# Performance work log

Measured on AMD Instinct MI355X. Metric: run time of the kernel, lower is better.

## Reference

```python
import jax, jax.numpy as jnp
import numpy as np

NOT_EPSILON = 1.0
W_SCALE = 0.05  # scaled randn init for numerical stability of swishmax logits

H, T, A, C = 8, 1024, 64, 256  # heads, key/query size, attention size, compress size


def swishmax(x, axis):
    m = jnp.max(x, axis=axis, keepdims=True)
    xe = x * jnp.exp(x - m)
    return xe / (jnp.sum(jnp.abs(xe), axis=axis, keepdims=True) + NOT_EPSILON)


def setup_inputs() -> dict:
    key = jax.random.key(0)
    ks = jax.random.split(key, 7)
    B, Q, K = 2, 2048, 2048
    return {
        "query_tokens": jax.random.normal(ks[0], (B, Q, T), dtype=jnp.float32),
        "key_tokens": jax.random.normal(ks[1], (B, K, T), dtype=jnp.float32),
        "key_down": jax.random.normal(ks[2], (H, T, A), dtype=jnp.float32) * W_SCALE,
        "query_down": jax.random.normal(ks[3], (H, T, A), dtype=jnp.float32) * W_SCALE,
        "query_down_bias": jax.random.normal(ks[4], (H, 1, A), dtype=jnp.float32) * W_SCALE,
        "value_down": jax.random.normal(ks[5], (H, T, C), dtype=jnp.float32) * W_SCALE,
        "value_up": jax.random.normal(ks[6], (H, C, T), dtype=jnp.float32) * W_SCALE,
    }


def reference(query_tokens, key_tokens, key_down, query_down, query_down_bias, value_down, value_up):
    # key/query projections: [B,K,T] x [H,T,A] -> [B,H,K,A]
    k = jnp.einsum('bkt,hta->bhka', key_tokens, key_down)
    q = jnp.einsum('bqt,hta->bhqa', query_tokens, query_down) + query_down_bias[None]  # [B,H,Q,A]
    # attention logits: key @ query^T -> [B,H,K,Q]
    logits = jnp.einsum('bhka,bhqa->bhkq', k, q)
    attn = swishmax(logits, axis=-2)  # normalized over keys (dim=-2)
    # sum_k key_tokens[b,k,:] * attn[b,h,k,q]  ==  [B,H,Q,T] (matmul form of the outer-product sum)
    vs = jnp.einsum('bhkq,bkt->bhqt', attn, key_tokens)
    # compress path: value_down then value_up
    vs = jnp.einsum('bhqc,hct->bhqt', jnp.einsum('bhqt,htc->bhqc', vs, value_down), value_up)
    return vs.sum(axis=1)  # sum over heads -> [B,Q,T]
```

## Files before the change

kernel.cpp:

```cpp
#include <hip/hip_runtime.h>
#include <hip/hip_fp16.h>
#include <math.h>


typedef _Float16 f16;
typedef _Float16 f16x4 __attribute__((ext_vector_type(4)));
typedef _Float16 f16x8 __attribute__((ext_vector_type(8)));
typedef short s16x4 __attribute__((ext_vector_type(4)));
typedef short bf16x8 __attribute__((ext_vector_type(8)));
typedef float f32x4 __attribute__((ext_vector_type(4)));

#define MFMA_F16(a, b, c) __builtin_amdgcn_mfma_f32_16x16x32_f16(a, b, c, 0, 0, 0)
#define MFMA_BF16(a, b, c) __builtin_amdgcn_mfma_f32_16x16x32_bf16(a, b, c, 0, 0, 0)

__device__ __forceinline__ void g2lds16(const void* g, void* l) {
  __builtin_amdgcn_global_load_lds((__attribute__((address_space(1))) void*)g,
                                   (__attribute__((address_space(3))) void*)l, 16, 0, 0);
}

__device__ __forceinline__ short f32_bf16(float x) {
  union { float f; unsigned u; } v; v.f = x;
  unsigned r = v.u + 0x7FFFu + ((v.u >> 16) & 1u);
  return (short)(r >> 16);
}
__device__ __forceinline__ float bf16_f32(short h) {
  union { unsigned u; float f; } v; v.u = ((unsigned)(unsigned short)h) << 16;
  return v.f;
}

__global__ __launch_bounds__(256) void ew_split2(const float* __restrict__ qin,
                                                 const float* __restrict__ kin,
                                                 short* __restrict__ qhi,
                                                 short* __restrict__ qlo,
                                                 short* __restrict__ khi,
                                                 short* __restrict__ klo,
                                                 f16* __restrict__ kf) {
  int i = blockIdx.x * 256 + threadIdx.x;
  const bool isK = i >= 1048576;
  const int j = isK ? i - 1048576 : i;
  const float* in = isK ? kin : qin;
  f32x4 v = ((const f32x4*)in)[j];
  s16x4 h, l;
  f16x4 f;
#pragma unroll
  for (int e = 0; e < 4; e++) {
    short he = f32_bf16(v[e]);
    h[e] = he;
    l[e] = f32_bf16(v[e] - bf16_f32(he));
    f[e] = (f16)v[e];
  }
  if (isK) {
    ((s16x4*)khi)[j] = h;
    ((s16x4*)klo)[j] = l;
    ((f16x4*)kf)[j] = f;
  } else {
    ((s16x4*)qhi)[j] = h;
    ((s16x4*)qlo)[j] = l;
  }
}

__global__ __launch_bounds__(256) void transpose_all(
    const float* __restrict__ qdw, const float* __restrict__ kdw,
    const float* __restrict__ vdw, const float* __restrict__ vup,
    short* __restrict__ wqT_hi, short* __restrict__ wqT_lo,
    short* __restrict__ wkT_hi, short* __restrict__ wkT_lo,
    f16* __restrict__ vdT, f16* __restrict__ vuT) {
  __shared__ float t[64][65];
  int idx = blockIdx.x;
  const float* in;
  short *bhi = nullptr, *blo = nullptr;
  f16* fo = nullptr;
  int R, C, cb, rb;
  size_t batch;
  if (idx < 256) {
    bool isQ = idx < 128;
    int i = isQ ? idx : idx - 128;
    in = isQ ? qdw : kdw;
    bhi = isQ ? wqT_hi : wkT_hi;
    blo = isQ ? wqT_lo : wkT_lo;
    R = 1024; C = 64; cb = 0; rb = (i & 15) * 64;
    batch = (size_t)(i >> 4) * R * C;
  } else if (idx < 768) {
    int i = idx - 256;
    in = vdw; fo = vdT;
    R = 1024; C = 256; cb = (i & 3) * 64; rb = ((i >> 2) & 15) * 64;
    batch = (size_t)(i >> 6) * R * C;
  } else {
    int i = idx - 768;
    in = vup; fo = vuT;
    R = 2048; C = 1024; cb = (i & 15) * 64; rb = (i >> 4) * 64;
    batch = 0;
  }
  int tid = threadIdx.x;
#pragma unroll
  for (int i = 0; i < 4; i++) {
    int r = (tid >> 4) + i * 16, c4 = (tid & 15) * 4;
    f32x4 v = *(const f32x4*)(in + batch + (size_t)(rb + r) * C + cb + c4);
    t[r][c4] = v[0]; t[r][c4 + 1] = v[1]; t[r][c4 + 2] = v[2]; t[r][c4 + 3] = v[3];
  }
  __syncthreads();
#pragma unroll
  for (int i = 0; i < 4; i++) {
    int c = (tid >> 4) + i * 16, r4 = (tid & 15) * 4;
    float v0 = t[r4][c], v1 = t[r4 + 1][c], v2 = t[r4 + 2][c], v3 = t[r4 + 3][c];
    size_t o = batch + (size_t)(cb + c) * R + rb + r4;
    if (bhi) {
      s16x4 h = {f32_bf16(v0), f32_bf16(v1), f32_bf16(v2), f32_bf16(v3)};
      *(s16x4*)(bhi + o) = h;
      s16x4 l = {f32_bf16(v0 - bf16_f32(h[0])), f32_bf16(v1 - bf16_f32(h[1])),
                 f32_bf16(v2 - bf16_f32(h[2])), f32_bf16(v3 - bf16_f32(h[3]))};
      *(s16x4*)(blo + o) = l;
    }
    if (fo) {
      f16x4 fv = {(f16)v0, (f16)v1, (f16)v2, (f16)v3};
      *(f16x4*)(fo + o) = fv;
    }
  }
}

__global__ __launch_bounds__(256, 3) void proj_gemm(
    const short* __restrict__ qtok_hi, const short* __restrict__ qtok_lo,
    const short* __restrict__ ktok_hi, const short* __restrict__ ktok_lo,
    const short* __restrict__ wqT_hi, const short* __restrict__ wqT_lo,
    const short* __restrict__ wkT_hi, const short* __restrict__ wkT_lo,
    const float* __restrict__ bias, short* __restrict__ q_split,
    short* __restrict__ k_split) {
  const bool isQ = (blockIdx.z == 0);
  const short* Ahi = isQ ? qtok_hi : ktok_hi;
  const short* Alo = isQ ? qtok_lo : ktok_lo;
  const short* Bhi = isQ ? wqT_hi : wkT_hi;
  const short* Blo = isQ ? wqT_lo : wkT_lo;
  short* outp = isQ ? q_split : k_split;

  __shared__ __attribute__((aligned(16))) short sm[2][12288];

  int tid = threadIdx.x, w = tid >> 6, lane = tid & 63, g = lane >> 4, li = lane & 15;
  int mb = blockIdx.y * 64, nb = blockIdx.x * 128;
  int wm = (w >> 1) * 32, wn = (w & 1) * 64;

  f32x4 acc[2][4] = {};

  auto STAGE = [&](int kb, int buf) {
    {
      int off = tid * 16;
      int row = off >> 6, ss = ((off >> 4) & 3) ^ ((row >> 1) & 3);
      size_t src = (size_t)(mb + row) * 1024 + kb + ss * 8;
      g2lds16(Ahi + src, (char*)&sm[buf][0] + w * 1024);
      g2lds16(Alo + src, (char*)&sm[buf][2048] + w * 1024);
    }
#pragma unroll
    for (int i = 0; i < 2; i++) {
      int off = i * 4096 + tid * 16;
      int row = off >> 6, ss = ((off >> 4) & 3) ^ ((row >> 1) & 3);
      size_t src = (size_t)(nb + row) * 1024 + kb + ss * 8;
      g2lds16(Bhi + src, (char*)&sm[buf][4096] + i * 4096 + w * 1024);
      g2lds16(Blo + src, (char*)&sm[buf][8192] + i * 4096 + w * 1024);
    }
  };

  STAGE(0, 0);
  __syncthreads();
  for (int kb = 0; kb < 1024; kb += 32) {
    int cur = (kb >> 5) & 1;
    if (kb + 32 < 1024) STAGE(kb + 32, cur ^ 1);
    bf16x8 af[2][2], bf[4][2];
#pragma unroll
    for (int f = 0; f < 2; f++) {
      int ra = wm + f * 16 + li, sa = g ^ ((ra >> 1) & 3);
      af[f][0] = *(const bf16x8*)&sm[cur][ra * 32 + sa * 8];
      af[f][1] = *(const bf16x8*)&sm[cur][2048 + ra * 32 + sa * 8];
    }
#pragma unroll
    for (int f = 0; f < 4; f++) {
      int rb = wn + f * 16 + li, sb = g ^ ((rb >> 1) & 3);
      bf[f][0] = *(const bf16x8*)&sm[cur][4096 + rb * 32 + sb * 8];
      bf[f][1] = *(const bf16x8*)&sm[cur][8192 + rb * 32 + sb * 8];
    }
#pragma unroll
    for (int mf = 0; mf < 2; mf++)
#pragma unroll
      for (int nf = 0; nf < 4; nf++) {
        acc[mf][nf] = MFMA_BF16(af[mf][0], bf[nf][0], acc[mf][nf]);
        acc[mf][nf] = MFMA_BF16(af[mf][0], bf[nf][1], acc[mf][nf]);
        acc[mf][nf] = MFMA_BF16(af[mf][1], bf[nf][0], acc[mf][nf]);
      }
    __syncthreads();
  }
#pragma unroll
  for (int mf = 0; mf < 2; mf++)
#pragma unroll
    for (int nf = 0; nf < 4; nf++)
#pragma unroll
      for (int r = 0; r < 4; r++) {
        int m = mb + wm + mf * 16 + 4 * g + r;
        int n = nb + wn + nf * 16 + li;
        float v = acc[mf][nf][r];
        if (isQ) v += bias[n];
        short hi = f32_bf16(v);
        short lo = f32_bf16(v - bf16_f32(hi));
        size_t base = ((size_t)((m >> 11) * 8 + (n >> 6)) * 2048 + (m & 2047)) * 128;
        outp[base + (n & 63)] = hi;
        outp[base + 64 + (n & 63)] = lo;
      }
}

__global__ __launch_bounds__(256, 4) void kv_gemm(const f16* __restrict__ A,
                                                  const f16* __restrict__ Bm,
                                                  f16* __restrict__ kvT) {
  __shared__ __attribute__((aligned(16))) f16 sm[2][6144];
  int tid = threadIdx.x, w = tid >> 6, lane = tid & 63, g = lane >> 4, li = lane & 15;
  int mb = blockIdx.y * 64, nb = blockIdx.x * 128;
  int wm = (w >> 1) * 32, wn = (w & 1) * 64;
  f32x4 acc[2][4] = {};

  auto STAGE = [&](int kb, int buf) {
    {
      int off = tid * 16;
      int row = off >> 6, ss = ((off >> 4) & 3) ^ ((row >> 1) & 3);
      g2lds16(A + (size_t)(mb + row) * 1024 + kb + ss * 8, (char*)&sm[buf][0] + w * 1024);
    }
#pragma unroll
    for (int i = 0; i < 2; i++) {
      int off = i * 4096 + tid * 16;
      int row = off >> 6, ss = ((off >> 4) & 3) ^ ((row >> 1) & 3);
      g2lds16(Bm + (size_t)(nb + row) * 1024 + kb + ss * 8,
              (char*)&sm[buf][2048] + i * 4096 + w * 1024);
    }
  };

  STAGE(0, 0);
  __syncthreads();
  for (int kb = 0; kb < 1024; kb += 32) {
    int cur = (kb >> 5) & 1;
    if (kb + 32 < 1024) STAGE(kb + 32, cur ^ 1);
    f16x8 af[2], bf[4];
#pragma unroll
    for (int f = 0; f < 2; f++) {
      int ra = wm + f * 16 + li, sa = g ^ ((ra >> 1) & 3);
      af[f] = *(const f16x8*)&sm[cur][ra * 32 + sa * 8];
    }
#pragma unroll
    for (int f = 0; f < 4; f++) {
      int rb = wn + f * 16 + li, sb = g ^ ((rb >> 1) & 3);
      bf[f] = *(const f16x8*)&sm[cur][2048 + rb * 32 + sb * 8];
    }
#pragma unroll
    for (int mf = 0; mf < 2; mf++)
#pragma unroll
      for (int nf = 0; nf < 4; nf++)
        acc[mf][nf] = MFMA_F16(af[mf], bf[nf], acc[mf][nf]);
    __syncthreads();
  }
#pragma unroll
  for (int mf = 0; mf < 2; mf++)
#pragma unroll
    for (int nf = 0; nf < 4; nf++) {
      int m = mb + wm + mf * 16 + 4 * g;
      int n = nb + wn + nf * 16 + li;
      f16x4 v = {(f16)acc[mf][nf][0], (f16)acc[mf][nf][1], (f16)acc[mf][nf][2],
                 (f16)acc[mf][nf][3]};
      int bh = (m >> 11) * 8 + (n >> 8);
      size_t o = (size_t)bh * 524288 + (size_t)((m & 2047) >> 5) * 8192 +
                 (size_t)(n & 255) * 32 + (m & 31);
      *(f16x4*)(kvT + o) = v;
    }
}

__global__ __launch_bounds__(256, 2) void flash_attn(const short* __restrict__ q_split,
                                                     const short* __restrict__ k_split,
                                                     const f16* __restrict__ kvT,
                                                     f16* __restrict__ vs_c) {
  __shared__ __attribute__((aligned(16))) short k_lds[2][8192];
  __shared__ __attribute__((aligned(16))) f16 p_lds[2][4096];
  __shared__ float sc_lds[2][4][16];
  __shared__ float fix_lds[64];

  const int bid = blockIdx.x;
  const int bh = ((bid & 7) << 1) + ((bid >> 3) & 1);
  const int qb = bid >> 4;
  const int tid = threadIdx.x;
  const int w = tid >> 6, lane = tid & 63, g = lane >> 4, li = lane & 15;

  const short* qrow = q_split + ((size_t)bh * 2048 + qb * 64 + w * 16 + li) * 128;
  bf16x8 qf[2][2];
#pragma unroll
  for (int ach = 0; ach < 2; ach++)
#pragma unroll
    for (int hl = 0; hl < 2; hl++)
      qf[ach][hl] = *(const bf16x8*)(qrow + hl * 64 + ach * 32 + g * 8);

  const short* kbase = k_split + (size_t)bh * 262144;
  const f16* kvbase = kvT + (size_t)bh * 524288 + (size_t)w * 64 * 32 + li * 32 + g * 8;

  float m_cur = -INFINITY, m_true = -INFINITY, l_run = 0.f;
  f32x4 acc[4][4] = {};
  f16x8 kvf[2][4];

  auto STAGE_K = [&](int t, int buf) {
#pragma unroll
    for (int i = 0; i < 4; i++) {
      int off = (w * 4 + i) * 1024 + lane * 16;
      int row = off >> 8;
      int ss = ((off >> 4) & 15) ^ (row & 7);
      g2lds16(kbase + t * 8192 + row * 128 + ss * 8,
              (char*)k_lds[buf] + (w * 4 + i) * 1024);
    }
  };

  auto LOADKV = [&](int t) {
#pragma unroll
    for (int h = 0; h < 2; h++) {
      const f16* p = kvbase + (size_t)(2 * t + h) * 8192;
#pragma unroll
      for (int ct = 0; ct < 4; ct++) kvf[h][ct] = *(const f16x8*)(p + ct * 512);
    }
  };

  auto QKSM = [&](int buf) {
    f32x4 s[4] = {};
    __builtin_amdgcn_s_setprio(1);
#pragma unroll
    for (int kc = 0; kc < 4; kc++) {
      const int r = kc * 16 + li;
#pragma unroll
      for (int ach = 0; ach < 2; ach++) {
        int sh = (ach * 4 + g) ^ (r & 7);
        int sl = (8 + ach * 4 + g) ^ (r & 7);
        bf16x8 khi = *(const bf16x8*)((const char*)k_lds[buf] + r * 256 + sh * 16);
        bf16x8 klo = *(const bf16x8*)((const char*)k_lds[buf] + r * 256 + sl * 16);
        s[kc] = MFMA_BF16(khi, qf[ach][0], s[kc]);
        s[kc] = MFMA_BF16(khi, qf[ach][1], s[kc]);
        s[kc] = MFMA_BF16(klo, qf[ach][0], s[kc]);
      }
    }
    __builtin_amdgcn_s_setprio(0);

    float tmax = -INFINITY;
#pragma unroll
    for (int kc = 0; kc < 4; kc++)
      tmax = fmaxf(tmax, fmaxf(fmaxf(s[kc][0], s[kc][1]), fmaxf(s[kc][2], s[kc][3])));
    tmax = fmaxf(tmax, __shfl_xor(tmax, 16));
    tmax = fmaxf(tmax, __shfl_xor(tmax, 32));
    m_true = fmaxf(m_true, tmax);
    float sc = 1.0f;
    if (__any(tmax > m_cur + 4.0f)) {
      float mn = fmaxf(m_cur, tmax);
      sc = __expf(m_cur - mn);
      l_run *= sc;
      m_cur = mn;
    }
    if (g == 0) sc_lds[buf][w][li] = sc;

    float ls = 0.f;
    float pv[16];
#pragma unroll
    for (int kc = 0; kc < 4; kc++)
#pragma unroll
      for (int r2 = 0; r2 < 4; r2++) {
        float sv = s[kc][r2];
        float e = sv * __expf(sv - m_cur);
        pv[kc * 4 + r2] = e;
        ls += fabsf(e);
      }
    ls += __shfl_xor(ls, 16);
    ls += __shfl_xor(ls, 32);
    l_run += ls;

#pragma unroll
    for (int kc = 0; kc < 4; kc++) {
      f16x4 p4 = {(f16)pv[kc * 4], (f16)pv[kc * 4 + 1], (f16)pv[kc * 4 + 2],
                  (f16)pv[kc * 4 + 3]};
      int wb = ((w * 16 + li) * 128 + kc * 32 + g * 8) ^ ((li & 7) << 4);
      *(f16x4*)((char*)p_lds[buf] + wb) = p4;
    }
  };

  STAGE_K(0, 0);
  STAGE_K(1, 1);
  __syncthreads();
  QKSM(0);

#pragma unroll 2
  for (int t = 0; t < 32; t++) {
    const int cur = t & 1;
    __syncthreads();
    LOADKV(t);
    if (t < 30) STAGE_K(t + 2, cur);
    if (t < 31) QKSM(cur ^ 1);

#pragma unroll
    for (int qt = 0; qt < 4; qt++) {
      float scq = sc_lds[cur][qt][li];
      if (__any(scq != 1.0f)) {
#pragma unroll
        for (int ct = 0; ct < 4; ct++) acc[ct][qt] *= scq;
      }
    }

    __builtin_amdgcn_s_setprio(1);
#pragma unroll
    for (int qt = 0; qt < 4; qt++) {
#pragma unroll
      for (int h = 0; h < 2; h++) {
        int rb = ((qt * 16 + li) * 128 + h * 64 + g * 16) ^ ((li & 7) << 4);
        f16x8 pf = *(const f16x8*)((const char*)p_lds[cur] + rb);
#pragma unroll
        for (int ct = 0; ct < 4; ct++)
          acc[ct][qt] = MFMA_F16(kvf[h][ct], pf, acc[ct][qt]);
      }
    }
    __builtin_amdgcn_s_setprio(0);
  }

  float sfix = __expf(m_cur - m_true);
  float invd = sfix / (l_run * sfix + 1.0f);
  __syncthreads();
  if (g == 0) fix_lds[w * 16 + li] = invd;
  __syncthreads();
#pragma unroll
  for (int qt = 0; qt < 4; qt++) {
    float iv = fix_lds[qt * 16 + li];
    f16* orow = vs_c + ((size_t)(bh >> 3) * 2048 + qb * 64 + qt * 16 + li) * 2048 +
                (bh & 7) * 256 + w * 64 + g * 4;
#pragma unroll
    for (int ct = 0; ct < 4; ct++) {
      f16x4 v = {(f16)(acc[ct][qt][0] * iv), (f16)(acc[ct][qt][1] * iv),
                 (f16)(acc[ct][qt][2] * iv), (f16)(acc[ct][qt][3] * iv)};
      *(f16x4*)(orow + ct * 16) = v;
    }
  }
}

__global__ __launch_bounds__(256, 4) void final_gemm(const f16* __restrict__ A,
                                                     const f16* __restrict__ Bm,
                                                     float* __restrict__ outp) {
  __shared__ __attribute__((aligned(16))) f16 sm[2][6144];
  int tid = threadIdx.x, w = tid >> 6, lane = tid & 63, g = lane >> 4, li = lane & 15;
  int mb = blockIdx.y * 64, nb = blockIdx.x * 128;
  int wm = (w >> 1) * 32, wn = (w & 1) * 64;
  f32x4 acc[2][4] = {};

  auto STAGE = [&](int kb, int buf) {
    {
      int off = tid * 16;
      int row = off >> 6, ss = ((off >> 4) & 3) ^ ((row >> 1) & 3);
      g2lds16(A + (size_t)(mb + row) * 2048 + kb + ss * 8, (char*)&sm[buf][0] + w * 1024);
    }
#pragma unroll
    for (int i = 0; i < 2; i++) {
      int off = i * 4096 + tid * 16;
      int row = off >> 6, ss = ((off >> 4) & 3) ^ ((row >> 1) & 3);
      g2lds16(Bm + (size_t)(nb + row) * 2048 + kb + ss * 8,
              (char*)&sm[buf][2048] + i * 4096 + w * 1024);
    }
  };

  STAGE(0, 0);
  __syncthreads();
  for (int kb = 0; kb < 2048; kb += 32) {
    int cur = (kb >> 5) & 1;
    if (kb + 32 < 2048) STAGE(kb + 32, cur ^ 1);
    f16x8 af[2], bf[4];
#pragma unroll
    for (int f = 0; f < 2; f++) {
      int ra = wm + f * 16 + li, sa = g ^ ((ra >> 1) & 3);
      af[f] = *(const f16x8*)&sm[cur][ra * 32 + sa * 8];
    }
#pragma unroll
    for (int f = 0; f < 4; f++) {
      int rb = wn + f * 16 + li, sb = g ^ ((rb >> 1) & 3);
      bf[f] = *(const f16x8*)&sm[cur][2048 + rb * 32 + sb * 8];
    }
#pragma unroll
    for (int mf = 0; mf < 2; mf++)
#pragma unroll
      for (int nf = 0; nf < 4; nf++)
        acc[mf][nf] = MFMA_F16(af[mf], bf[nf], acc[mf][nf]);
    __syncthreads();
  }
#pragma unroll
  for (int mf = 0; mf < 2; mf++)
#pragma unroll
    for (int nf = 0; nf < 4; nf++)
#pragma unroll
      for (int r = 0; r < 4; r++) {
        int m = mb + wm + mf * 16 + 4 * g + r;
        int n = nb + wn + nf * 16 + li;
        outp[(size_t)m * 1024 + n] = acc[mf][nf][r];
      }
}

extern "C" void kernel_launch(void* const* d_in, const int* in_sizes, int n_in,
                              void* d_out, int out_size, void* d_ws, size_t ws_size,
                              hipStream_t stream) {
  (void)in_sizes; (void)n_in; (void)out_size; (void)ws_size;
  const float* qtok = (const float*)d_in[0];
  const float* ktok = (const float*)d_in[1];
  const float* kdw = (const float*)d_in[2];
  const float* qdw = (const float*)d_in[3];
  const float* qdb = (const float*)d_in[4];
  const float* vdw = (const float*)d_in[5];
  const float* vup = (const float*)d_in[6];

  char* ws = (char*)d_ws;
  size_t off = 0;
  auto take = [&](size_t n) { void* p = ws + off; off += (n + 255) & ~(size_t)255; return p; };

  short* qtok_hi = (short*)take(8u << 20);
  short* qtok_lo = (short*)take(8u << 20);
  short* ktok_hi = (short*)take(8u << 20);
  short* ktok_lo = (short*)take(8u << 20);
  f16* ktok_f = (f16*)take(8u << 20);
  short* wqT_hi = (short*)take(1u << 20);
  short* wqT_lo = (short*)take(1u << 20);
  short* wkT_hi = (short*)take(1u << 20);
  short* wkT_lo = (short*)take(1u << 20);
  f16* vdT = (f16*)take(4u << 20);
  f16* vuT = (f16*)take(4u << 20);
  short* q_split = (short*)take(8u << 20);
  short* k_split = (short*)take(8u << 20);
  f16* kvT = (f16*)(void*)ktok_hi;
  f16* vs_c = (f16*)(void*)qtok_hi;

  ew_split2<<<8192, 256, 0, stream>>>(qtok, ktok, qtok_hi, qtok_lo, ktok_hi,
                                      ktok_lo, ktok_f);
  transpose_all<<<1280, 256, 0, stream>>>(qdw, kdw, vdw, vup, wqT_hi, wqT_lo,
                                          wkT_hi, wkT_lo, vdT, vuT);
  proj_gemm<<<dim3(4, 64, 2), 256, 0, stream>>>(qtok_hi, qtok_lo, ktok_hi, ktok_lo,
                                                wqT_hi, wqT_lo, wkT_hi, wkT_lo, qdb,
                                                q_split, k_split);
  kv_gemm<<<dim3(16, 64), 256, 0, stream>>>(ktok_f, vdT, kvT);
  flash_attn<<<512, 256, 0, stream>>>(q_split, k_split, kvT, vs_c);
  final_gemm<<<dim3(8, 64), 256, 0, stream>>>(vs_c, vuT, (float*)d_out);
}
```

Baseline: 203.9 us.

## Warp-specialize flash_attn into QK/softmax and PV waves with 512 threads

Splits the attention block into two wave groups: four waves compute QK logits and swishmax probabilities into LDS, while four other waves stage K tiles and run the P·KV MFMA accumulation. The aim is to overlap the softmax/QK phase with the PV phase across wave groups instead of serializing them within each wave. The block grows to 512 threads with launch bounds (512,4), which tightens register budgets and may cause spills. It also relies on the existing double-buffered LDS sync for correctness between producer and consumer waves.

```diff
diff --git a/kernel.cpp b/kernel.cpp
--- a/kernel.cpp
+++ b/kernel.cpp
@@ -266,7 +266,7 @@
     }
 }
 
-__global__ __launch_bounds__(256, 2) void flash_attn(const short* __restrict__ q_split,
+__global__ __launch_bounds__(512, 4) void flash_attn(const short* __restrict__ q_split,
                                                      const short* __restrict__ k_split,
                                                      const f16* __restrict__ kvT,
                                                      f16* __restrict__ vs_c) {
@@ -280,39 +280,33 @@
   const int qb = bid >> 4;
   const int tid = threadIdx.x;
   const int w = tid >> 6, lane = tid & 63, g = lane >> 4, li = lane & 15;
-
-  const short* qrow = q_split + ((size_t)bh * 2048 + qb * 64 + w * 16 + li) * 128;
+  const bool isQK = (w < 4);
+  const int wp = w & 3;
+
+  const short* kbase = k_split + (size_t)bh * 262144;
+
   bf16x8 qf[2][2];
-#pragma unroll
-  for (int ach = 0; ach < 2; ach++)
-#pragma unroll
-    for (int hl = 0; hl < 2; hl++)
-      qf[ach][hl] = *(const bf16x8*)(qrow + hl * 64 + ach * 32 + g * 8);
-
-  const short* kbase = k_split + (size_t)bh * 262144;
-  const f16* kvbase = kvT + (size_t)bh * 524288 + (size_t)w * 64 * 32 + li * 32 + g * 8;
-
   float m_cur = -INFINITY, m_true = -INFINITY, l_run = 0.f;
+  if (isQK) {
+    const short* qrow = q_split + ((size_t)bh * 2048 + qb * 64 + wp * 16 + li) * 128;
+#pragma unroll
+    for (int ach = 0; ach < 2; ach++)
+#pragma unroll
+      for (int hl = 0; hl < 2; hl++)
+        qf[ach][hl] = *(const bf16x8*)(qrow + hl * 64 + ach * 32 + g * 8);
+  }
+
+  const f16* kvbase = kvT + (size_t)bh * 524288 + (size_t)wp * 2048 + li * 32 + g * 8;
   f32x4 acc[4][4] = {};
-  f16x8 kvf[2][4];
 
   auto STAGE_K = [&](int t, int buf) {
 #pragma unroll
     for (int i = 0; i < 4; i++) {
-      int off = (w * 4 + i) * 1024 + lane * 16;
+      int off = (wp * 4 + i) * 1024 + lane * 16;
       int row = off >> 8;
       int ss = ((off >> 4) & 15) ^ (row & 7);
       g2lds16(kbase + t * 8192 + row * 128 + ss * 8,
-              (char*)k_lds[buf] + (w * 4 + i) * 1024);
-    }
-  };
-
-  auto LOADKV = [&](int t) {
-#pragma unroll
-    for (int h = 0; h < 2; h++) {
-      const f16* p = kvbase + (size_t)(2 * t + h) * 8192;
-#pragma unroll
-      for (int ct = 0; ct < 4; ct++) kvf[h][ct] = *(const f16x8*)(p + ct * 512);
+              (char*)k_lds[buf] + (wp * 4 + i) * 1024);
     }
   };
 
@@ -349,7 +343,7 @@
       l_run *= sc;
       m_cur = mn;
     }
-    if (g == 0) sc_lds[buf][w][li] = sc;
+    if (g == 0) sc_lds[buf][wp][li] = sc;
 
     float ls = 0.f;
     float pv[16];
@@ -370,63 +364,72 @@
     for (int kc = 0; kc < 4; kc++) {
       f16x4 p4 = {(f16)pv[kc * 4], (f16)pv[kc * 4 + 1], (f16)pv[kc * 4 + 2],
                   (f16)pv[kc * 4 + 3]};
-      int wb = ((w * 16 + li) * 128 + kc * 32 + g * 8) ^ ((li & 7) << 4);
+      int wb = ((wp * 16 + li) * 128 + kc * 32 + g * 8) ^ ((li & 7) << 4);
       *(f16x4*)((char*)p_lds[buf] + wb) = p4;
     }
   };
 
-  STAGE_K(0, 0);
-  STAGE_K(1, 1);
+  if (!isQK) {
+    STAGE_K(0, 0);
+    STAGE_K(1, 1);
+  }
   __syncthreads();
-  QKSM(0);
+  if (isQK) QKSM(0);
 
 #pragma unroll 2
   for (int t = 0; t < 32; t++) {
     const int cur = t & 1;
     __syncthreads();
-    LOADKV(t);
-    if (t < 30) STAGE_K(t + 2, cur);
-    if (t < 31) QKSM(cur ^ 1);
-
+    if (isQK) {
+      if (t < 31) QKSM(cur ^ 1);
+    } else {
+      if (t < 30) STAGE_K(t + 2, cur);
+#pragma unroll
+      for (int qt = 0; qt < 4; qt++) {
+        float scq = sc_lds[cur][qt][li];
+        if (__any(scq != 1.0f)) {
+#pragma unroll
+          for (int ct = 0; ct < 4; ct++) acc[ct][qt] *= scq;
+        }
+      }
+#pragma unroll
+      for (int h = 0; h < 2; h++) {
+        f16x8 kvf[4];
+        const f16* p = kvbase + (size_t)(2 * t + h) * 8192;
+#pragma unroll
+        for (int ct = 0; ct < 4; ct++) kvf[ct] = *(const f16x8*)(p + ct * 512);
+        __builtin_amdgcn_s_setprio(1);
+#pragma unroll
+        for (int qt = 0; qt < 4; qt++) {
+          int rb = ((qt * 16 + li) * 128 + h * 64 + g * 16) ^ ((li & 7) << 4);
+          f16x8 pf = *(const f16x8*)((const char*)p_lds[cur] + rb);
+#pragma unroll
+          for (int ct = 0; ct < 4; ct++)
+            acc[ct][qt] = MFMA_F16(kvf[ct], pf, acc[ct][qt]);
+        }
+        __builtin_amdgcn_s_setprio(0);
+      }
+    }
+  }
+
+  if (isQK) {
+    float sfix = __expf(m_cur - m_true);
+    float invd = sfix / (l_run * sfix + 1.0f);
+    if (g == 0) fix_lds[wp * 16 + li] = invd;
+  }
+  __syncthreads();
+  if (!isQK) {
 #pragma unroll
     for (int qt = 0; qt < 4; qt++) {
-      float scq = sc_lds[cur][qt][li];
-      if (__any(scq != 1.0f)) {
-#pragma unroll
-        for (int ct = 0; ct < 4; ct++) acc[ct][qt] *= scq;
-      }
-    }
-
-    __builtin_amdgcn_s_setprio(1);
-#pragma unroll
-    for (int qt = 0; qt < 4; qt++) {
-#pragma unroll
-      for (int h = 0; h < 2; h++) {
-        int rb = ((qt * 16 + li) * 128 + h * 64 + g * 16) ^ ((li & 7) << 4);
-        f16x8 pf = *(const f16x8*)((const char*)p_lds[cur] + rb);
-#pragma unroll
-        for (int ct = 0; ct < 4; ct++)
-          acc[ct][qt] = MFMA_F16(kvf[h][ct], pf, acc[ct][qt]);
-      }
-    }
-    __builtin_amdgcn_s_setprio(0);
-  }
-
-  float sfix = __expf(m_cur - m_true);
-  float invd = sfix / (l_run * sfix + 1.0f);
-  __syncthreads();
-  if (g == 0) fix_lds[w * 16 + li] = invd;
-  __syncthreads();
-#pragma unroll
-  for (int qt = 0; qt < 4; qt++) {
-    float iv = fix_lds[qt * 16 + li];
-    f16* orow = vs_c + ((size_t)(bh >> 3) * 2048 + qb * 64 + qt * 16 + li) * 2048 +
-                (bh & 7) * 256 + w * 64 + g * 4;
-#pragma unroll
-    for (int ct = 0; ct < 4; ct++) {
-      f16x4 v = {(f16)(acc[ct][qt][0] * iv), (f16)(acc[ct][qt][1] * iv),
-                 (f16)(acc[ct][qt][2] * iv), (f16)(acc[ct][qt][3] * iv)};
-      *(f16x4*)(orow + ct * 16) = v;
+      float iv = fix_lds[qt * 16 + li];
+      f16* orow = vs_c + ((size_t)(bh >> 3) * 2048 + qb * 64 + qt * 16 + li) * 2048 +
+                  (bh & 7) * 256 + wp * 64 + g * 4;
+#pragma unroll
+      for (int ct = 0; ct < 4; ct++) {
+        f16x4 v = {(f16)(acc[ct][qt][0] * iv), (f16)(acc[ct][qt][1] * iv),
+                   (f16)(acc[ct][qt][2] * iv), (f16)(acc[ct][qt][3] * iv)};
+        *(f16x4*)(orow + ct * 16) = v;
+      }
     }
   }
 }
@@ -530,6 +533,6 @@
                                                 wqT_hi, wqT_lo, wkT_hi, wkT_lo, qdb,
                                                 q_split, k_split);
   kv_gemm<<<dim3(16, 64), 256, 0, stream>>>(ktok_f, vdT, kvT);
-  flash_attn<<<512, 256, 0, stream>>>(q_split, k_split, kvT, vs_c);
+  flash_attn<<<512, 512, 0, stream>>>(q_split, k_split, kvT, vs_c);
   final_gemm<<<dim3(8, 64), 256, 0, stream>>>(vs_c, vuT, (float*)d_out);
 }
```

Result: slower. 240.8 us (+18.1%).

## Split flash attention over key halves and merge partials in combine kernel

Applied to the files above, without the earlier changes.

Splits the flash attention key range into two halves processed by separate blocks, doubling the grid from 512 to 1024 blocks, and raises the launch bound occupancy target from 2 to 3. Each half writes a normalized partial output plus per-query sum and max statistics, and a new combine_halves kernel merges the two partials with the swishmax +1 denominator. The aim is to fill more compute units on the MI355X. The cost is an extra kernel launch, extra global traffic for the second partial buffer, and possible register spilling under the tighter launch bound.

```diff
diff --git a/kernel.cpp b/kernel.cpp
--- a/kernel.cpp
+++ b/kernel.cpp
@@ -266,18 +266,23 @@
     }
 }
 
-__global__ __launch_bounds__(256, 2) void flash_attn(const short* __restrict__ q_split,
+__global__ __launch_bounds__(256, 3) void flash_attn(const short* __restrict__ q_split,
                                                      const short* __restrict__ k_split,
                                                      const f16* __restrict__ kvT,
-                                                     f16* __restrict__ vs_c) {
+                                                     f16* __restrict__ P0,
+                                                     f16* __restrict__ P1,
+                                                     float* __restrict__ Lm,
+                                                     float* __restrict__ Mm) {
   __shared__ __attribute__((aligned(16))) short k_lds[2][8192];
   __shared__ __attribute__((aligned(16))) f16 p_lds[2][4096];
   __shared__ float sc_lds[2][4][16];
   __shared__ float fix_lds[64];
 
   const int bid = blockIdx.x;
-  const int bh = ((bid & 7) << 1) + ((bid >> 3) & 1);
-  const int qb = bid >> 4;
+  const int kb2 = bid & 1;
+  const int r_ = bid >> 1;
+  const int bh = ((r_ & 7) << 1) + ((r_ >> 3) & 1);
+  const int qb = r_ >> 4;
   const int tid = threadIdx.x;
   const int w = tid >> 6, lane = tid & 63, g = lane >> 4, li = lane & 15;
 
@@ -289,8 +294,9 @@
     for (int hl = 0; hl < 2; hl++)
       qf[ach][hl] = *(const bf16x8*)(qrow + hl * 64 + ach * 32 + g * 8);
 
-  const short* kbase = k_split + (size_t)bh * 262144;
-  const f16* kvbase = kvT + (size_t)bh * 524288 + (size_t)w * 64 * 32 + li * 32 + g * 8;
+  const short* kbase = k_split + (size_t)bh * 262144 + (size_t)kb2 * 131072;
+  const f16* kvbase = kvT + (size_t)bh * 524288 + (size_t)kb2 * 262144 +
+                      (size_t)w * 2048 + li * 32 + g * 8;
 
   float m_cur = -INFINITY, m_true = -INFINITY, l_run = 0.f;
   f32x4 acc[4][4] = {};
@@ -381,12 +387,12 @@
   QKSM(0);
 
 #pragma unroll 2
-  for (int t = 0; t < 32; t++) {
+  for (int t = 0; t < 16; t++) {
     const int cur = t & 1;
     __syncthreads();
     LOADKV(t);
-    if (t < 30) STAGE_K(t + 2, cur);
-    if (t < 31) QKSM(cur ^ 1);
+    if (t < 14) STAGE_K(t + 2, cur);
+    if (t < 15) QKSM(cur ^ 1);
 
 #pragma unroll
     for (int qt = 0; qt < 4; qt++) {
@@ -415,12 +421,18 @@
   float sfix = __expf(m_cur - m_true);
   float invd = sfix / (l_run * sfix + 1.0f);
   __syncthreads();
-  if (g == 0) fix_lds[w * 16 + li] = invd;
-  __syncthreads();
+  if (g == 0) {
+    fix_lds[w * 16 + li] = invd;
+    int qg = qb * 64 + w * 16 + li;
+    Lm[(size_t)kb2 * 32768 + bh * 2048 + qg] = l_run * sfix;
+    Mm[(size_t)kb2 * 32768 + bh * 2048 + qg] = m_true;
+  }
+  __syncthreads();
+  f16* Pb = kb2 ? P1 : P0;
 #pragma unroll
   for (int qt = 0; qt < 4; qt++) {
     float iv = fix_lds[qt * 16 + li];
-    f16* orow = vs_c + ((size_t)(bh >> 3) * 2048 + qb * 64 + qt * 16 + li) * 2048 +
+    f16* orow = Pb + ((size_t)(bh >> 3) * 2048 + qb * 64 + qt * 16 + li) * 2048 +
                 (bh & 7) * 256 + w * 64 + g * 4;
 #pragma unroll
     for (int ct = 0; ct < 4; ct++) {
@@ -429,6 +441,31 @@
       *(f16x4*)(orow + ct * 16) = v;
     }
   }
+}
+
+__global__ __launch_bounds__(256) void combine_halves(const f16* __restrict__ p1,
+                                                      f16* __restrict__ p0io,
+                                                      const float* __restrict__ Lm,
+                                                      const float* __restrict__ Mm) {
+  size_t i = (size_t)blockIdx.x * 256 + threadIdx.x;
+  size_t lin8 = i * 8;
+  int batch = (int)(lin8 >> 22);
+  int q = (int)((lin8 >> 11) & 2047);
+  int h = (int)((lin8 & 2047) >> 8);
+  int s = (batch * 8 + h) * 2048 + q;
+  float L0 = Lm[s], L1 = Lm[32768 + s];
+  float M0 = Mm[s], M1 = Mm[32768 + s];
+  float M = fmaxf(M0, M1);
+  float w0 = __expf(M0 - M), w1 = __expf(M1 - M);
+  float a0 = (L0 + 1.0f) * w0, a1 = (L1 + 1.0f) * w1;
+  float invd = 1.0f / (L0 * w0 + L1 * w1 + 1.0f);
+  f16x8 v0 = *(const f16x8*)(p0io + lin8);
+  f16x8 v1 = *(const f16x8*)(p1 + lin8);
+  f16x8 o;
+#pragma unroll
+  for (int e = 0; e < 8; e++)
+    o[e] = (f16)(((float)v0[e] * a0 + (float)v1[e] * a1) * invd);
+  *(f16x8*)(p0io + lin8) = o;
 }
 
 __global__ __launch_bounds__(256, 4) void final_gemm(const f16* __restrict__ A,
@@ -519,8 +556,11 @@
   f16* vuT = (f16*)take(4u << 20);
   short* q_split = (short*)take(8u << 20);
   short* k_split = (short*)take(8u << 20);
+  float* Lm = (float*)take(256u << 10);
+  float* Mm = (float*)take(256u << 10);
   f16* kvT = (f16*)(void*)ktok_hi;
   f16* vs_c = (f16*)(void*)qtok_hi;
+  f16* P1 = (f16*)(void*)ktok_f;
 
   ew_split2<<<8192, 256, 0, stream>>>(qtok, ktok, qtok_hi, qtok_lo, ktok_hi,
                                       ktok_lo, ktok_f);
@@ -530,6 +570,7 @@
                                                 wqT_hi, wqT_lo, wkT_hi, wkT_lo, qdb,
                                                 q_split, k_split);
   kv_gemm<<<dim3(16, 64), 256, 0, stream>>>(ktok_f, vdT, kvT);
-  flash_attn<<<512, 256, 0, stream>>>(q_split, k_split, kvT, vs_c);
+  flash_attn<<<1024, 256, 0, stream>>>(q_split, k_split, kvT, vs_c, P1, Lm, Mm);
+  combine_halves<<<4096, 256, 0, stream>>>(P1, vs_c, Lm, Mm);
   final_gemm<<<dim3(8, 64), 256, 0, stream>>>(vs_c, vuT, (float*)d_out);
 }
```

Result: slower. 321.3 us (+57.6%).
